# Performance work log

Hardware: AMD Instinct MI355X
Metric: run time of the kernel (lower is better)

Reference implementation:

```python
import jax, jax.numpy as jnp
import numpy as np

E = 8        # number of sessions (experts)
N = 512      # per-session input width (max units)
P = 512      # n_channels (output width)
F = 100      # max_F time bins
B = 128      # batch of trials
SCALE = 1.0


def setup_inputs() -> dict:
    key = jax.random.key(0)
    kx, ke, k1, k2, k3, k4 = jax.random.split(key, 6)
    x = jax.random.normal(kx, (B, F, N), dtype=jnp.float32)
    eid = jax.random.randint(ke, (B,), 0, E, dtype=jnp.int32)
    # Per-session stitcher Linear(N, 2N) and projector Linear(2N, P), stacked.
    s1 = 1.0 / np.sqrt(N)
    s2 = 1.0 / np.sqrt(2 * N)
    W1 = jax.random.uniform(k1, (E, N, 2 * N), jnp.float32, -s1, s1)
    b1 = jax.random.uniform(k2, (E, 2 * N), jnp.float32, -s1, s1)
    W2 = jax.random.uniform(k3, (E, 2 * N, P), jnp.float32, -s2, s2)
    b2 = jax.random.uniform(k4, (E, P), jnp.float32, -s2, s2)
    return {"x": x, "eid": eid, "W1": W1, "b1": b1, "W2": W2, "b2": b2}


def reference(x, eid, W1, b1, W2, b2):
    # Grouped (per-session) Linear -> Softsign -> Linear, dispatched by eid.
    # Equivalent to the torch loop over unique eids with mask gather/scatter,
    # expressed as a gather of per-sample expert weights + batched matmul.
    w1 = W1[eid]                      # [B, N, 2N]
    stitched = jnp.einsum('bfn,bnh->bfh', x, w1) + b1[eid][:, None, :]
    act = stitched / (1.0 + jnp.abs(stitched))  # Softsign
    act = act * SCALE
    w2 = W2[eid]                      # [B, 2N, P]
    out = jnp.einsum('bfh,bhp->bfp', act, w2) + b2[eid][:, None, :]
    return out                        # [B, F, P]
```

## Files before the change

kernel.cpp:

```cpp
#include <hip/hip_runtime.h>
#include <hip/hip_bf16.h>

#define B_ 128
#define F_ 100
#define N_ 512
#define H_ 1024
#define P_ 512
#define E_ 8

#define BM 128
#define BK 64

typedef __attribute__((ext_vector_type(8))) short bf16x8;
typedef __attribute__((ext_vector_type(4))) float f32x4;

#define GLOAD16(g, l) __builtin_amdgcn_global_load_lds(                      \
    (const __attribute__((address_space(1))) void*)(g),                      \
    (__attribute__((address_space(3))) void*)(l), 16, 0, 0)

static __device__ __forceinline__ short f2bf(float f) {
    __hip_bfloat16 h = __float2bfloat16(f);
    short s;
    __builtin_memcpy(&s, &h, sizeof(s));
    return s;
}

__global__ __launch_bounds__(256) void convert_x(const float* __restrict__ x,
                                                 short* __restrict__ xbf) {
    const int g = blockIdx.x * 256 + threadIdx.x;
    const int col = (g & (N_ / 8 - 1)) * 8;
    const int row = g >> 6;
    const int f = row & 127, b = row >> 7;
    union { short s[8]; uint4 u; } o;
    if (f < F_) {
        const float* xp = x + ((size_t)(b * F_ + f)) * N_ + col;
        const float4 v0 = *(const float4*)(xp);
        const float4 v1 = *(const float4*)(xp + 4);
        o.s[0] = f2bf(v0.x); o.s[1] = f2bf(v0.y);
        o.s[2] = f2bf(v0.z); o.s[3] = f2bf(v0.w);
        o.s[4] = f2bf(v1.x); o.s[5] = f2bf(v1.y);
        o.s[6] = f2bf(v1.z); o.s[7] = f2bf(v1.w);
    } else {
        o.u = make_uint4(0u, 0u, 0u, 0u);
    }
    *(uint4*)(xbf + (size_t)row * N_ + col) = o.u;
}

__global__ __launch_bounds__(256) void transpose_cvt(const float* __restrict__ W,
                                                     short* __restrict__ WT,
                                                     int R, int C) {
    __shared__ float tile[64][65];
    const int e = blockIdx.z;
    const int c0 = blockIdx.x * 64, r0 = blockIdx.y * 64;
    const int t = threadIdx.x;
    const float* Wp = W + (size_t)e * R * C;
    short* WTp = WT + (size_t)e * C * R;
    {
        const int c4 = (t & 15) * 4, r = t >> 4;
#pragma unroll
        for (int p = 0; p < 4; p++) {
            const int row = p * 16 + r;
            const float4 v = *(const float4*)(Wp + (size_t)(r0 + row) * C + c0 + c4);
            tile[row][c4 + 0] = v.x; tile[row][c4 + 1] = v.y;
            tile[row][c4 + 2] = v.z; tile[row][c4 + 3] = v.w;
        }
    }
    __syncthreads();
    {
        const int r8 = (t & 7) * 8, cl = t >> 3;
#pragma unroll
        for (int p = 0; p < 2; p++) {
            const int c = p * 32 + cl;
            union { short s[8]; uint4 u; } o;
#pragma unroll
            for (int j = 0; j < 8; j++) o.s[j] = f2bf(tile[r8 + j][c]);
            *(uint4*)(&WTp[(size_t)(c0 + c) * R + r0 + r8]) = o.u;
        }
    }
}

template <int KDIM, int BN_, bool FIRST>
__global__ __launch_bounds__(256, 4) void gemm_kernel(
    const short* __restrict__ A,
    const short* __restrict__ WT,
    const float* __restrict__ bias,
    const int* __restrict__ eid,
    short* __restrict__ actout,
    float* __restrict__ out)
{
    constexpr int NCOLS = FIRST ? H_ : P_;
    constexpr int NI = BN_ / 32;
    __shared__ short sA[BM * BK];
    __shared__ short sB[BN_ * BK];
    const int b = blockIdx.y;
    const int n0 = blockIdx.x * BN_;
    const int e = eid[b];
    const int t = threadIdx.x;
    const int lane = t & 63, w = t >> 6;
    const int wm = (w >> 1) * 64, wn = (w & 1) * (BN_ / 2);
    const int l15 = lane & 15, quad = lane >> 4;
    const int lr = lane >> 3, lc = (lane & 7) * 8;

    f32x4 acc[4][NI];
#pragma unroll
    for (int mi = 0; mi < 4; mi++)
#pragma unroll
        for (int ni = 0; ni < NI; ni++)
            acc[mi][ni] = (f32x4)(0.0f);

    const short* Ap = A + (size_t)b * BM * KDIM;
    const short* Bp = WT + ((size_t)e * NCOLS + n0) * KDIM;

    for (int k0 = 0; k0 < KDIM; k0 += BK) {
#pragma unroll
        for (int i = 0; i < 4; i++) {
            const int rb = w * 32 + i * 8;
            GLOAD16(Ap + (size_t)(rb + lr) * KDIM + k0 + lc, &sA[rb * BK]);
        }
#pragma unroll
        for (int i = 0; i < BN_ / 32; i++) {
            const int rb = w * (BN_ / 4) + i * 8;
            GLOAD16(Bp + (size_t)(rb + lr) * KDIM + k0 + lc, &sB[rb * BK]);
        }
        __syncthreads();
#pragma unroll
        for (int ks = 0; ks < 2; ks++) {
            bf16x8 af[4], bfr[NI];
#pragma unroll
            for (int mi = 0; mi < 4; mi++)
                af[mi] = *(const bf16x8*)(&sA[(wm + mi * 16 + l15) * BK + ks * 32 + quad * 8]);
#pragma unroll
            for (int ni = 0; ni < NI; ni++)
                bfr[ni] = *(const bf16x8*)(&sB[(wn + ni * 16 + l15) * BK + ks * 32 + quad * 8]);
#pragma unroll
            for (int mi = 0; mi < 4; mi++)
#pragma unroll
                for (int ni = 0; ni < NI; ni++)
                    acc[mi][ni] = __builtin_amdgcn_mfma_f32_16x16x32_bf16(af[mi], bfr[ni], acc[mi][ni], 0, 0, 0);
        }
        __syncthreads();
    }

#pragma unroll
    for (int mi = 0; mi < 4; mi++) {
#pragma unroll
        for (int ni = 0; ni < NI; ni++) {
            const int col = n0 + wn + ni * 16 + l15;
            const float bv = bias[(size_t)e * NCOLS + col];
#pragma unroll
            for (int r = 0; r < 4; r++) {
                const int row = wm + mi * 16 + quad * 4 + r;
                float v = acc[mi][ni][r] + bv;
                if constexpr (FIRST) {
                    v = v / (1.0f + fabsf(v));
                    actout[((size_t)b * BM + row) * H_ + col] = f2bf(v);
                } else {
                    if (row < F_)
                        out[((size_t)b * F_ + row) * P_ + col] = v;
                }
            }
        }
    }
}

extern "C" void kernel_launch(void* const* d_in, const int* in_sizes, int n_in,
                              void* d_out, int out_size, void* d_ws, size_t ws_size,
                              hipStream_t stream) {
    const float* x  = (const float*)d_in[0];
    const int* eid  = (const int*)d_in[1];
    const float* W1 = (const float*)d_in[2];
    const float* b1 = (const float*)d_in[3];
    const float* W2 = (const float*)d_in[4];
    const float* b2 = (const float*)d_in[5];
    float* out = (float*)d_out;

    char* ws = (char*)d_ws;
    short* W1T = (short*)(ws);
    short* W2T = (short*)(ws + (size_t)(8u << 20));
    short* act = (short*)(ws + (size_t)(16u << 20));
    short* xbf = (short*)(ws + (size_t)(48u << 20));

    convert_x<<<dim3((B_ * 128 * N_ / 8) / 256), 256, 0, stream>>>(x, xbf);
    transpose_cvt<<<dim3(H_ / 64, N_ / 64, E_), 256, 0, stream>>>(W1, W1T, N_, H_);
    transpose_cvt<<<dim3(P_ / 64, H_ / 64, E_), 256, 0, stream>>>(W2, W2T, H_, P_);
    gemm_kernel<N_, 128, true><<<dim3(H_ / 128, B_), 256, 0, stream>>>(xbf, W1T, b1, eid, act, nullptr);
    gemm_kernel<H_, 64, false><<<dim3(P_ / 64, B_), 256, 0, stream>>>(act, W2T, b2, eid, nullptr, out);
}
```

Baseline: 185.4 us.

## Sort samples by expert, remap grid across XCDs, and XOR-swizzle LDS tiles

```diff
diff --git a/kernel.cpp b/kernel.cpp
--- a/kernel.cpp
+++ b/kernel.cpp
@@ -25,14 +25,36 @@
     return s;
 }
 
+__global__ __launch_bounds__(128) void sort_eid(const int* __restrict__ eid,
+                                                int* __restrict__ perm,
+                                                int* __restrict__ esort) {
+    __shared__ int cnt[E_], base[E_];
+    const int t = threadIdx.x;
+    if (t < E_) cnt[t] = 0;
+    __syncthreads();
+    const int e = eid[t];
+    atomicAdd(&cnt[e], 1);
+    __syncthreads();
+    if (t == 0) {
+        int s = 0;
+        for (int i = 0; i < E_; i++) { base[i] = s; s += cnt[i]; }
+    }
+    __syncthreads();
+    const int pos = atomicAdd(&base[e], 1);
+    perm[pos] = t;
+    esort[pos] = e;
+}
+
 __global__ __launch_bounds__(256) void convert_x(const float* __restrict__ x,
-                                                 short* __restrict__ xbf) {
+                                                 const int* __restrict__ perm,
+                                                 short* __restrict__ xs) {
     const int g = blockIdx.x * 256 + threadIdx.x;
     const int col = (g & (N_ / 8 - 1)) * 8;
     const int row = g >> 6;
-    const int f = row & 127, b = row >> 7;
+    const int f = row & 127, sp = row >> 7;
     union { short s[8]; uint4 u; } o;
     if (f < F_) {
+        const int b = perm[sp];
         const float* xp = x + ((size_t)(b * F_ + f)) * N_ + col;
         const float4 v0 = *(const float4*)(xp);
         const float4 v1 = *(const float4*)(xp + 4);
@@ -43,7 +65,7 @@
     } else {
         o.u = make_uint4(0u, 0u, 0u, 0u);
     }
-    *(uint4*)(xbf + (size_t)row * N_ + col) = o.u;
+    *(uint4*)(xs + (size_t)row * N_ + col) = o.u;
 }
 
 __global__ __launch_bounds__(256) void transpose_cvt(const float* __restrict__ W,
@@ -84,7 +106,8 @@
     const short* __restrict__ A,
     const short* __restrict__ WT,
     const float* __restrict__ bias,
-    const int* __restrict__ eid,
+    const int* __restrict__ perm,
+    const int* __restrict__ esort,
     short* __restrict__ actout,
     float* __restrict__ out)
 {
@@ -92,14 +115,15 @@
     constexpr int NI = BN_ / 32;
     __shared__ short sA[BM * BK];
     __shared__ short sB[BN_ * BK];
-    const int b = blockIdx.y;
-    const int n0 = blockIdx.x * BN_;
-    const int e = eid[b];
+    const int sp = (blockIdx.x & 7) * 16 + (blockIdx.x >> 3);
+    const int n0 = blockIdx.y * BN_;
+    const int e = esort[sp];
     const int t = threadIdx.x;
     const int lane = t & 63, w = t >> 6;
     const int wm = (w >> 1) * 64, wn = (w & 1) * (BN_ / 2);
     const int l15 = lane & 15, quad = lane >> 4;
-    const int lr = lane >> 3, lc = (lane & 7) * 8;
+    const int lr = lane >> 3;
+    const int lc = (((lane & 7) ^ lr) * 8);
 
     f32x4 acc[4][NI];
 #pragma unroll
@@ -108,7 +132,7 @@
         for (int ni = 0; ni < NI; ni++)
             acc[mi][ni] = (f32x4)(0.0f);
 
-    const short* Ap = A + (size_t)b * BM * KDIM;
+    const short* Ap = A + (size_t)sp * BM * KDIM;
     const short* Bp = WT + ((size_t)e * NCOLS + n0) * KDIM;
 
     for (int k0 = 0; k0 < KDIM; k0 += BK) {
@@ -127,11 +151,15 @@
         for (int ks = 0; ks < 2; ks++) {
             bf16x8 af[4], bfr[NI];
 #pragma unroll
-            for (int mi = 0; mi < 4; mi++)
-                af[mi] = *(const bf16x8*)(&sA[(wm + mi * 16 + l15) * BK + ks * 32 + quad * 8]);
-#pragma unroll
-            for (int ni = 0; ni < NI; ni++)
-                bfr[ni] = *(const bf16x8*)(&sB[(wn + ni * 16 + l15) * BK + ks * 32 + quad * 8]);
+            for (int mi = 0; mi < 4; mi++) {
+                const int ra = wm + mi * 16 + l15;
+                af[mi] = *(const bf16x8*)(&sA[ra * BK + (((ks * 4 + quad) ^ (ra & 7)) * 8)]);
+            }
+#pragma unroll
+            for (int ni = 0; ni < NI; ni++) {
+                const int rbn = wn + ni * 16 + l15;
+                bfr[ni] = *(const bf16x8*)(&sB[rbn * BK + (((ks * 4 + quad) ^ (rbn & 7)) * 8)]);
+            }
 #pragma unroll
             for (int mi = 0; mi < 4; mi++)
 #pragma unroll
@@ -141,6 +169,7 @@
         __syncthreads();
     }
 
+    const int borig = FIRST ? 0 : perm[sp];
 #pragma unroll
     for (int mi = 0; mi < 4; mi++) {
 #pragma unroll
@@ -153,10 +182,10 @@
                 float v = acc[mi][ni][r] + bv;
                 if constexpr (FIRST) {
                     v = v / (1.0f + fabsf(v));
-                    actout[((size_t)b * BM + row) * H_ + col] = f2bf(v);
+                    actout[((size_t)sp * BM + row) * H_ + col] = f2bf(v);
                 } else {
                     if (row < F_)
-                        out[((size_t)b * F_ + row) * P_ + col] = v;
+                        out[((size_t)borig * F_ + row) * P_ + col] = v;
                 }
             }
         }
@@ -178,11 +207,14 @@
     short* W1T = (short*)(ws);
     short* W2T = (short*)(ws + (size_t)(8u << 20));
     short* act = (short*)(ws + (size_t)(16u << 20));
-    short* xbf = (short*)(ws + (size_t)(48u << 20));
-
-    convert_x<<<dim3((B_ * 128 * N_ / 8) / 256), 256, 0, stream>>>(x, xbf);
+    short* xs  = (short*)(ws + (size_t)(48u << 20));
+    int* perm  = (int*)(ws + (size_t)(64u << 20));
+    int* esort = perm + B_;
+
+    sort_eid<<<1, 128, 0, stream>>>(eid, perm, esort);
+    convert_x<<<dim3((B_ * 128 * N_ / 8) / 256), 256, 0, stream>>>(x, perm, xs);
     transpose_cvt<<<dim3(H_ / 64, N_ / 64, E_), 256, 0, stream>>>(W1, W1T, N_, H_);
     transpose_cvt<<<dim3(P_ / 64, H_ / 64, E_), 256, 0, stream>>>(W2, W2T, H_, P_);
-    gemm_kernel<N_, 128, true><<<dim3(H_ / 128, B_), 256, 0, stream>>>(xbf, W1T, b1, eid, act, nullptr);
-    gemm_kernel<H_, 64, false><<<dim3(P_ / 64, B_), 256, 0, stream>>>(act, W2T, b2, eid, nullptr, out);
-}
+    gemm_kernel<N_, 128, true><<<dim3(B_, H_ / 128), 256, 0, stream>>>(xs, W1T, b1, perm, esort, act, nullptr);
+    gemm_kernel<H_, 64, false><<<dim3(B_, P_ / 64), 256, 0, stream>>>(act, W2T, b2, perm, esort, nullptr, out);
+}
```

Result: faster. 158.3 us (-14.6%).
